# Performance work log

Measured on AMD Instinct MI355X. Metric: run time of the kernel, lower is better.

Reference implementation:

```python
import jax, jax.numpy as jnp
import numpy as np

N_NODES = 100000
N_EDGES = 1600000
K = 48

def setup_inputs() -> dict:
    key = jax.random.key(0)
    ks = jax.random.split(key, 6)
    x = jax.random.normal(ks[0], (N_NODES, K), dtype=jnp.float32)
    pos_edge_index = jax.random.randint(ks[1], (2, N_EDGES), 0, N_NODES, dtype=jnp.int64)
    neg_edge_index = jax.random.randint(ks[2], (2, N_EDGES), 0, N_NODES, dtype=jnp.int64)
    # nn.Linear-style init (uniform +-1/sqrt(fan_in))
    lim1 = 1.0 / np.sqrt(3 * K)
    W1 = jax.random.uniform(ks[3], (3 * K, 16), minval=-lim1, maxval=lim1, dtype=jnp.float32)
    b1 = jnp.zeros((16,), dtype=jnp.float32)
    lim2 = 1.0 / np.sqrt(16)
    W2 = jax.random.uniform(ks[4], (16, K), minval=-lim2, maxval=lim2, dtype=jnp.float32)
    b2 = jnp.zeros((K,), dtype=jnp.float32)
    return {"x": x, "pos_edge_index": pos_edge_index, "neg_edge_index": neg_edge_index,
            "W1": W1, "b1": b1, "W2": W2, "b2": b2}

def _scatter_add_mp(x, edge_index):
    # PyG MessagePassing(aggr='add'), message = x_j:
    # gather source-node features and scatter-add into target nodes.
    src, dst = edge_index[0], edge_index[1]
    msgs = x[src]  # [E, k]
    return jax.ops.segment_sum(msgs, dst, num_segments=x.shape[0])  # [N, k]

def reference(x, pos_edge_index, neg_edge_index, W1, b1, W2, b2):
    x_pos = _scatter_add_mp(x, pos_edge_index)
    x_neg = _scatter_add_mp(x, neg_edge_index)
    out_cat = jnp.concatenate([x, x_pos, x_neg], axis=1)  # [N, 3k]
    h = jnp.tanh(out_cat @ W1 + b1)                        # [N, 16]
    C = h @ W2 + b2                                        # [N, k]
    return jax.nn.softmax(C, axis=1)
```

## Files before the change

kernel.cpp:

```cpp
#include <hip/hip_runtime.h>
#include <hip/hip_fp16.h>
#include <math.h>

#define NN 100000
#define NE 1600000
#define KF 48
#define NEDGE_ALL (2 * NE)

#define BKT_NODES 128
#define NBKT_PER  782
#define NBKT      1564
#define PACK_EPB  4096
#define NPB       782
#define OT2       1566
#define CAP2      2432
#define KSTG      10

typedef _Float16 half2v __attribute__((ext_vector_type(2)));
typedef _Float16 half4v __attribute__((ext_vector_type(4)));
typedef _Float16 half8v __attribute__((ext_vector_type(8)));

#if defined(__has_builtin)
#if __has_builtin(__builtin_amdgcn_fdot2)
#define HAVE_FDOT2 1
#endif
#endif

__device__ __forceinline__ void acc_pair(float& ax, float& ay, half2v v)
{
#ifdef HAVE_FDOT2
    ax = __builtin_amdgcn_fdot2(v, (half2v){(_Float16)1.f, (_Float16)0.f}, ax, false);
    ay = __builtin_amdgcn_fdot2(v, (half2v){(_Float16)0.f, (_Float16)1.f}, ay, false);
#else
    ax += (float)v.x;
    ay += (float)v.y;
#endif
}

__global__ __launch_bounds__(512) void pack_kernel(
    const float* __restrict__ x,
    const int* __restrict__ ei_pos,
    const int* __restrict__ ei_neg,
    const float* __restrict__ W1,
    const float* __restrict__ b1,
    unsigned short* __restrict__ offT,
    unsigned* __restrict__ plist,
    float* __restrict__ za,
    __half* __restrict__ zbh,
    __half* __restrict__ zch)
{
    __shared__ int cnt[NBKT];
    __shared__ int ps[391];
    __shared__ unsigned stage[PACK_EPB];
    __shared__ float sW1[144 * 16];
    __shared__ float sb1[16];

    const int t = threadIdx.x;
    for (int i = t; i < 144 * 16; i += 512) sW1[i] = W1[i];
    if (t < 16) sb1[t] = b1[t];
    for (int i = t; i < NBKT; i += 512) cnt[i] = 0;
    __syncthreads();

    {
        const int n = blockIdx.x * 512 + t;
        if (n < NN + 2) {
            float aA[16], aB[16], aC[16];
#pragma unroll
            for (int j = 0; j < 16; ++j) { aA[j] = sb1[j]; aB[j] = 0.f; aC[j] = 0.f; }
            if (n < NN) {
                const float4* __restrict__ x4 = (const float4*)(x + (long)n * KF);
                for (int i4 = 0; i4 < 12; ++i4) {
                    float4 v = x4[i4];
                    float vv[4] = {v.x, v.y, v.z, v.w};
#pragma unroll
                    for (int c = 0; c < 4; ++c) {
                        const int f = i4 * 4 + c;
                        const float* wA = &sW1[f * 16];
                        const float* wB = &sW1[(48 + f) * 16];
                        const float* wC = &sW1[(96 + f) * 16];
                        const float s = vv[c];
#pragma unroll
                        for (int j = 0; j < 16; ++j) {
                            aA[j] += s * wA[j];
                            aB[j] += s * wB[j];
                            aC[j] += s * wC[j];
                        }
                    }
                }
                float4* za4 = (float4*)(za + (long)n * 16);
#pragma unroll
                for (int j4 = 0; j4 < 4; ++j4)
                    za4[j4] = make_float4(aA[4*j4], aA[4*j4+1], aA[4*j4+2], aA[4*j4+3]);
            }
            half8v hb0, hb1, hc0, hc1;
#pragma unroll
            for (int j = 0; j < 8; ++j) {
                hb0[j] = (_Float16)aB[j];     hb1[j] = (_Float16)aB[8 + j];
                hc0[j] = (_Float16)aC[j];     hc1[j] = (_Float16)aC[8 + j];
            }
            half8v* zb8 = (half8v*)zbh;
            half8v* zc8 = (half8v*)zch;
            zb8[(long)n * 2 + 0] = hb0;  zb8[(long)n * 2 + 1] = hb1;
            zc8[(long)n * 2 + 0] = hc0;  zc8[(long)n * 2 + 1] = hc1;
        }
    }

    unsigned pk[8];
    int bk[8];
    const int blockBase = blockIdx.x * PACK_EPB;
#pragma unroll
    for (int j = 0; j < 8; ++j) {
        int e = blockBase + j * 512 + t;
        bk[j] = -1;
        if (e < NEDGE_ALL) {
            int list = e >= NE;
            int ee = list ? e - NE : e;
            const int* ei = list ? ei_neg : ei_pos;
            int src = ei[ee];
            int dst = ei[NE + ee];
            int b = list * NBKT_PER + (dst >> 7);
            bk[j] = b;
            pk[j] = ((unsigned)(dst & 127) << 17) | (unsigned)src;
            atomicAdd(&cnt[b], 1);
        }
    }
    __syncthreads();

    int s0 = 0, s1 = 0, s2 = 0, s3 = 0;
    if (t < 391) {
        s0 = cnt[4 * t]; s1 = cnt[4 * t + 1]; s2 = cnt[4 * t + 2]; s3 = cnt[4 * t + 3];
        ps[t] = s0 + s1 + s2 + s3;
    }
    __syncthreads();
    for (int d = 1; d < 391; d <<= 1) {
        int v = (t < 391 && t >= d) ? ps[t - d] : 0;
        __syncthreads();
        if (t < 391) ps[t] += v;
        __syncthreads();
    }
    unsigned short* myrow = offT + (long)blockIdx.x * OT2;
    if (t < 391) {
        int base = t ? ps[t - 1] : 0;
        int o0 = base, o1 = o0 + s0, o2 = o1 + s1, o3 = o2 + s2;
        myrow[4 * t]     = (unsigned short)o0;
        myrow[4 * t + 1] = (unsigned short)o1;
        myrow[4 * t + 2] = (unsigned short)o2;
        myrow[4 * t + 3] = (unsigned short)o3;
        cnt[4 * t] = o0; cnt[4 * t + 1] = o1; cnt[4 * t + 2] = o2; cnt[4 * t + 3] = o3;
    }
    if (t == 390) myrow[NBKT] = (unsigned short)ps[390];
    __syncthreads();

#pragma unroll
    for (int j = 0; j < 8; ++j) {
        if (bk[j] >= 0) {
            int slot = atomicAdd(&cnt[bk[j]], 1);
            stage[slot] = pk[j];
        }
    }
    __syncthreads();

    {
        const uint4* __restrict__ st4 = (const uint4*)stage;
        uint4* __restrict__ out4 = (uint4*)(plist + (long)blockIdx.x * PACK_EPB);
#pragma unroll
        for (int j = 0; j < 2; ++j)
            out4[j * 512 + t] = st4[j * 512 + t];
    }
}

__global__ __launch_bounds__(256) void gather_kernel(
    const __half* __restrict__ zbh,
    const __half* __restrict__ zch,
    const unsigned* __restrict__ plist,
    const unsigned short* __restrict__ offT,
    float* __restrict__ hpos,
    float* __restrict__ hneg)
{
    __shared__ unsigned srt[CAP2];
    __shared__ int rb[NPB + 2];
    __shared__ unsigned short rsL[NPB];
    __shared__ int tmp[196];
    __shared__ int nh[BKT_NODES];
    __shared__ int starts[BKT_NODES];
    __shared__ int ends[BKT_NODES];
    __shared__ int cur2[BKT_NODES];

    const int b = blockIdx.x;
    const int t = threadIdx.x;

    for (int r = t; r < NPB; r += 256) {
        int s = offT[(long)r * OT2 + b];
        int e = offT[(long)r * OT2 + b + 1];
        rsL[r] = (unsigned short)s;
        srt[r] = (unsigned)(e - s);
    }
    if (t < BKT_NODES) nh[t] = 0;
    __syncthreads();

    int s0 = 0, s1 = 0, s2 = 0, s3 = 0;
    if (t < 196) {
        int i0 = 4 * t;
        s0 = (i0     < NPB) ? (int)srt[i0]     : 0;
        s1 = (i0 + 1 < NPB) ? (int)srt[i0 + 1] : 0;
        s2 = (i0 + 2 < NPB) ? (int)srt[i0 + 2] : 0;
        s3 = (i0 + 3 < NPB) ? (int)srt[i0 + 3] : 0;
        tmp[t] = s0 + s1 + s2 + s3;
    }
    __syncthreads();
    for (int d = 1; d < 196; d <<= 1) {
        int v = (t < 196 && t >= d) ? tmp[t - d] : 0;
        __syncthreads();
        if (t < 196) tmp[t] += v;
        __syncthreads();
    }
    if (t < 196) {
        int base = t ? tmp[t - 1] : 0;
        int i0 = 4 * t;
        if (i0     <= NPB) rb[i0]     = base;
        if (i0 + 1 <= NPB) rb[i0 + 1] = base + s0;
        if (i0 + 2 <= NPB) rb[i0 + 2] = base + s0 + s1;
        if (i0 + 3 <= NPB) rb[i0 + 3] = base + s0 + s1 + s2;
    }
    __syncthreads();
    int cb = rb[NPB];
    if (cb > CAP2) cb = CAP2;

    unsigned held[KSTG];
#pragma unroll
    for (int k = 0; k < KSTG; ++k) {
        int i = t + k * 256;
        held[k] = 0;
        if (i < cb) {
            int lo = 0, hi = NPB - 1;
#pragma unroll
            for (int it = 0; it < 10; ++it) {
                int mid = (lo + hi + 1) >> 1;
                bool ge = (rb[mid] <= i);
                lo = ge ? mid : lo;
                hi = ge ? hi : mid - 1;
            }
            unsigned p = plist[(long)lo * PACK_EPB + rsL[lo] + (i - rb[lo])];
            held[k] = p;
            atomicAdd(&nh[p >> 17], 1);
        }
    }
    __syncthreads();

    for (int d = 1; d < BKT_NODES; d <<= 1) {
        int v = 0;
        if (t < BKT_NODES && t >= d) v = nh[t - d];
        __syncthreads();
        if (t < BKT_NODES) nh[t] += v;
        __syncthreads();
    }
    if (t < BKT_NODES) {
        int e_ = min(nh[t], CAP2);
        int s_ = t ? min(nh[t - 1], CAP2) : 0;
        starts[t] = s_;
        ends[t] = e_;
        cur2[t] = s_;
    }
    __syncthreads();

#pragma unroll
    for (int k = 0; k < KSTG; ++k) {
        int i = t + k * 256;
        if (i < cb) {
            unsigned p = held[k];
            int slot = atomicAdd(&cur2[p >> 17], 1);
            if (slot < CAP2) srt[slot] = p;
        }
    }
    __syncthreads();

    const int wave = t >> 6, lane = t & 63;
    const int g = lane >> 2;
    const int sub = lane & 3;
    const int list = b >= NBKT_PER;
    const int nb = list ? b - NBKT_PER : b;
    float* o = list ? hneg : hpos;
    const half4v* __restrict__ z4 = (const half4v*)(list ? zch : zbh);

    for (int n = wave; n < BKT_NODES; n += 4) {
        int gn = nb * BKT_NODES + n;
        if (gn >= NN) continue;
        int s = starts[n], e = ends[n];
        float a0 = 0.f, a1 = 0.f, a2 = 0.f, a3 = 0.f;
        for (int j = s; j < e; j += 16) {
            int i0 = j + g;
            int q = (i0 < e) ? (int)(srt[i0 < CAP2 ? i0 : 0] & 0x1FFFFu) : NN;
            half4v v = z4[q * 4 + sub];
            acc_pair(a0, a1, (half2v){v.x, v.y});
            acc_pair(a2, a3, (half2v){v.z, v.w});
        }
        a0 += __shfl_xor(a0, 4); a0 += __shfl_xor(a0, 8); a0 += __shfl_xor(a0, 16); a0 += __shfl_xor(a0, 32);
        a1 += __shfl_xor(a1, 4); a1 += __shfl_xor(a1, 8); a1 += __shfl_xor(a1, 16); a1 += __shfl_xor(a1, 32);
        a2 += __shfl_xor(a2, 4); a2 += __shfl_xor(a2, 8); a2 += __shfl_xor(a2, 16); a2 += __shfl_xor(a2, 32);
        a3 += __shfl_xor(a3, 4); a3 += __shfl_xor(a3, 8); a3 += __shfl_xor(a3, 16); a3 += __shfl_xor(a3, 32);
        if (g == 0) {
            float4* o4 = (float4*)o;
            o4[(long)gn * 4 + sub] = make_float4(a0, a1, a2, a3);
        }
    }
}

__global__ __launch_bounds__(256) void mlp2_kernel(
    const float* __restrict__ za,
    const float* __restrict__ hpos,
    const float* __restrict__ hneg,
    const float* __restrict__ W2,
    const float* __restrict__ b2,
    float* __restrict__ out)
{
    __shared__ float sW2[16 * 48];
    __shared__ float sb2[48];
    for (int i = threadIdx.x; i < 16 * 48; i += 256) sW2[i] = W2[i];
    if (threadIdx.x < 48) sb2[threadIdx.x] = b2[threadIdx.x];
    __syncthreads();

    const int n = blockIdx.x * 256 + threadIdx.x;
    if (n >= NN) return;

    const float4* A = (const float4*)(za   + (long)n * 16);
    const float4* P = (const float4*)(hpos + (long)n * 16);
    const float4* Q = (const float4*)(hneg + (long)n * 16);
    float h[16];
#pragma unroll
    for (int j4 = 0; j4 < 4; ++j4) {
        float4 a = A[j4], p = P[j4], q = Q[j4];
        h[4 * j4 + 0] = tanhf(a.x + p.x + q.x);
        h[4 * j4 + 1] = tanhf(a.y + p.y + q.y);
        h[4 * j4 + 2] = tanhf(a.z + p.z + q.z);
        h[4 * j4 + 3] = tanhf(a.w + p.w + q.w);
    }

    float C[KF];
#pragma unroll
    for (int k = 0; k < KF; ++k) C[k] = sb2[k];
    for (int j = 0; j < 16; ++j) {
        const float hv = h[j];
        const float* w = &sW2[j * KF];
#pragma unroll
        for (int k = 0; k < KF; ++k) C[k] += hv * w[k];
    }

    float m = C[0];
#pragma unroll
    for (int k = 1; k < KF; ++k) m = fmaxf(m, C[k]);
    float ssum = 0.f;
#pragma unroll
    for (int k = 0; k < KF; ++k) { C[k] = expf(C[k] - m); ssum += C[k]; }
    const float inv = 1.0f / ssum;

    float4* po = (float4*)(out + (long)n * KF);
#pragma unroll
    for (int k4 = 0; k4 < 12; ++k4)
        po[k4] = make_float4(C[4*k4] * inv, C[4*k4+1] * inv, C[4*k4+2] * inv, C[4*k4+3] * inv);
}

__global__ __launch_bounds__(256) void scatter2_kernel(
    const float* __restrict__ x,
    const int* __restrict__ ei_pos,
    const int* __restrict__ ei_neg,
    float* acc_pos,
    float* acc_neg)
{
    const int list = blockIdx.y;
    const int* ei = list ? ei_neg : ei_pos;
    float* acc = list ? acc_neg : acc_pos;

    long t = (long)blockIdx.x * blockDim.x + threadIdx.x;
    const long total = (long)NE * 12;
    if (t >= total) return;

    int e = (int)(t / 12);
    int r = (int)(t - (long)e * 12);
    int k4 = r * 4;

    int src = ei[e];
    int dst = ei[NE + e];

    const float4 v = *(const float4*)(x + (long)src * KF + k4);
    float* p = acc + (long)dst * KF + k4;

    unsafeAtomicAdd(p + 0, v.x);
    unsafeAtomicAdd(p + 1, v.y);
    unsafeAtomicAdd(p + 2, v.z);
    unsafeAtomicAdd(p + 3, v.w);
}

__global__ __launch_bounds__(256) void mlp_softmax_kernel(
    const float* __restrict__ x,
    const float* xpos,
    const float* __restrict__ xneg,
    const float* __restrict__ W1,
    const float* __restrict__ b1,
    const float* __restrict__ W2,
    const float* __restrict__ b2,
    float* out)
{
    __shared__ float sW1[144 * 16];
    __shared__ float sW2[16 * 48];
    __shared__ float sb1[16];
    __shared__ float sb2[48];

    for (int i = threadIdx.x; i < 144 * 16; i += blockDim.x) sW1[i] = W1[i];
    for (int i = threadIdx.x; i < 16 * 48;  i += blockDim.x) sW2[i] = W2[i];
    if (threadIdx.x < 16) sb1[threadIdx.x] = b1[threadIdx.x];
    if (threadIdx.x < 48) sb2[threadIdx.x] = b2[threadIdx.x];
    __syncthreads();

    const int n = blockIdx.x * blockDim.x + threadIdx.x;
    if (n >= NN) return;

    float h[16];
#pragma unroll
    for (int j = 0; j < 16; ++j) h[j] = sb1[j];

    const float* srcs[3];
    srcs[0] = x    + (long)n * KF;
    srcs[1] = xpos + (long)n * KF;
    srcs[2] = xneg + (long)n * KF;

    for (int s = 0; s < 3; ++s) {
        const float* px = srcs[s];
        for (int i = 0; i < KF; ++i) {
            const float v = px[i];
            const float* w = &sW1[(s * KF + i) * 16];
#pragma unroll
            for (int j = 0; j < 16; ++j) h[j] += v * w[j];
        }
    }
#pragma unroll
    for (int j = 0; j < 16; ++j) h[j] = tanhf(h[j]);

    float C[KF];
#pragma unroll
    for (int k = 0; k < KF; ++k) C[k] = sb2[k];
    for (int j = 0; j < 16; ++j) {
        const float hv = h[j];
        const float* w = &sW2[j * KF];
#pragma unroll
        for (int k = 0; k < KF; ++k) C[k] += hv * w[k];
    }

    float m = C[0];
#pragma unroll
    for (int k = 1; k < KF; ++k) m = fmaxf(m, C[k]);
    float ssum = 0.f;
#pragma unroll
    for (int k = 0; k < KF; ++k) { C[k] = expf(C[k] - m); ssum += C[k]; }
    const float inv = 1.0f / ssum;

    float* po = out + (long)n * KF;
#pragma unroll
    for (int k = 0; k < KF; ++k) po[k] = C[k] * inv;
}

extern "C" void kernel_launch(void* const* d_in, const int* in_sizes, int n_in,
                              void* d_out, int out_size, void* d_ws, size_t ws_size,
                              hipStream_t stream)
{
    const float* x      = (const float*)d_in[0];
    const int*   ei_pos = (const int*)  d_in[1];
    const int*   ei_neg = (const int*)  d_in[2];
    const float* W1     = (const float*)d_in[3];
    const float* b1     = (const float*)d_in[4];
    const float* W2     = (const float*)d_in[5];
    const float* b2     = (const float*)d_in[6];

    float* out = (float*)d_out;

    const size_t h_bytes     = (size_t)NN * 16 * sizeof(float);
    const size_t za_bytes    = (size_t)NN * 16 * sizeof(float);
    const size_t zh_bytes    = (size_t)(NN + 2) * 16 * sizeof(__half);
    const size_t plist_bytes = (size_t)NPB * PACK_EPB * sizeof(unsigned);
    const size_t offT_bytes  = (size_t)NPB * OT2 * sizeof(unsigned short);

    size_t off = 0;
    char* ws = (char*)d_ws;
    float*          hpos  = (float*)(ws + off);          off += h_bytes;
    float*          hneg  = (float*)(ws + off);          off += h_bytes;
    float*          za    = (float*)(ws + off);          off += za_bytes;
    __half*         zbh   = (__half*)(ws + off);         off += zh_bytes;
    __half*         zch   = (__half*)(ws + off);         off += zh_bytes;
    unsigned*       plist = (unsigned*)(ws + off);       off += plist_bytes;
    unsigned short* offT  = (unsigned short*)(ws + off); off += offT_bytes;
    const size_t needed = off;

    if (ws_size >= needed) {
        pack_kernel<<<NPB, 512, 0, stream>>>(x, ei_pos, ei_neg, W1, b1, offT, plist, za, zbh, zch);
        gather_kernel<<<NBKT, 256, 0, stream>>>(zbh, zch, plist, offT, hpos, hneg);
        mlp2_kernel<<<(NN + 255) / 256, 256, 0, stream>>>(za, hpos, hneg, W2, b2, out);
    } else {
        float* xpos = (float*)d_out;
        float* xneg = (float*)d_ws;
        const size_t acc_bytes = (size_t)NN * KF * sizeof(float);
        hipMemsetAsync(xpos, 0, acc_bytes, stream);
        hipMemsetAsync(xneg, 0, acc_bytes, stream);
        const long total = (long)NE * 12;
        dim3 grid((unsigned)((total + 255) / 256), 2, 1);
        scatter2_kernel<<<grid, 256, 0, stream>>>(x, ei_pos, ei_neg, xpos, xneg);
        mlp_softmax_kernel<<<(NN + 255) / 256, 256, 0, stream>>>(x, xpos, xneg, W1, b1, W2, b2, out);
    }
}
```

Baseline: 204.2 us.

## Pack 16K edges per block to shrink per-bucket offset table rows

The pack kernel now handles 16384 edges per block instead of 4096, so there are 196 pack blocks rather than 782. Because the staging buffer would not fit in LDS, it is written out in two halves. The gather kernel now reads 196 offset rows per bucket instead of 782, which simplifies its prefix scan and shortens its binary search. In exchange, each pack block holds 32 edges per thread in registers, issues more LDS atomics, and adds extra barriers. Fewer pack blocks may also leave the GPU underused, and offsets stored as unsigned short could overflow if one bucket's count within a block reached 65536.

```diff
diff --git a/kernel.cpp b/kernel.cpp
--- a/kernel.cpp
+++ b/kernel.cpp
@@ -10,8 +10,9 @@
 #define BKT_NODES 128
 #define NBKT_PER  782
 #define NBKT      1564
-#define PACK_EPB  4096
-#define NPB       782
+#define PACK_EPB  16384
+#define STG_HALF  8192
+#define NPB       196
 #define OT2       1566
 #define CAP2      2432
 #define KSTG      10
@@ -51,7 +52,7 @@
 {
     __shared__ int cnt[NBKT];
     __shared__ int ps[391];
-    __shared__ unsigned stage[PACK_EPB];
+    __shared__ unsigned stage[STG_HALF];
     __shared__ float sW1[144 * 16];
     __shared__ float sb1[16];
 
@@ -105,11 +106,11 @@
         }
     }
 
-    unsigned pk[8];
-    int bk[8];
+    unsigned pk[32];
+    int bk[32];
     const int blockBase = blockIdx.x * PACK_EPB;
 #pragma unroll
-    for (int j = 0; j < 8; ++j) {
+    for (int j = 0; j < 32; ++j) {
         int e = blockBase + j * 512 + t;
         bk[j] = -1;
         if (e < NEDGE_ALL) {
@@ -152,19 +153,37 @@
     __syncthreads();
 
 #pragma unroll
-    for (int j = 0; j < 8; ++j) {
-        if (bk[j] >= 0) {
-            int slot = atomicAdd(&cnt[bk[j]], 1);
-            stage[slot] = pk[j];
-        }
-    }
-    __syncthreads();
-
+    for (int j = 0; j < 32; ++j) {
+        if (bk[j] >= 0)
+            bk[j] = atomicAdd(&cnt[bk[j]], 1);
+    }
+
+#pragma unroll
+    for (int j = 0; j < 32; ++j) {
+        if (bk[j] >= 0 && bk[j] < STG_HALF)
+            stage[bk[j]] = pk[j];
+    }
+    __syncthreads();
     {
         const uint4* __restrict__ st4 = (const uint4*)stage;
         uint4* __restrict__ out4 = (uint4*)(plist + (long)blockIdx.x * PACK_EPB);
 #pragma unroll
-        for (int j = 0; j < 2; ++j)
+        for (int j = 0; j < 4; ++j)
+            out4[j * 512 + t] = st4[j * 512 + t];
+    }
+    __syncthreads();
+
+#pragma unroll
+    for (int j = 0; j < 32; ++j) {
+        if (bk[j] >= STG_HALF)
+            stage[bk[j] - STG_HALF] = pk[j];
+    }
+    __syncthreads();
+    {
+        const uint4* __restrict__ st4 = (const uint4*)stage;
+        uint4* __restrict__ out4 = (uint4*)(plist + (long)blockIdx.x * PACK_EPB + STG_HALF);
+#pragma unroll
+        for (int j = 0; j < 4; ++j)
             out4[j * 512 + t] = st4[j * 512 + t];
     }
 }
@@ -179,8 +198,8 @@
 {
     __shared__ unsigned srt[CAP2];
     __shared__ int rb[NPB + 2];
+    __shared__ int sc[NPB];
     __shared__ unsigned short rsL[NPB];
-    __shared__ int tmp[196];
     __shared__ int nh[BKT_NODES];
     __shared__ int starts[BKT_NODES];
     __shared__ int ends[BKT_NODES];
@@ -189,39 +208,23 @@
     const int b = blockIdx.x;
     const int t = threadIdx.x;
 
-    for (int r = t; r < NPB; r += 256) {
-        int s = offT[(long)r * OT2 + b];
-        int e = offT[(long)r * OT2 + b + 1];
-        rsL[r] = (unsigned short)s;
-        srt[r] = (unsigned)(e - s);
+    if (t < NPB) {
+        int s = offT[(long)t * OT2 + b];
+        int e = offT[(long)t * OT2 + b + 1];
+        rsL[t] = (unsigned short)s;
+        sc[t] = e - s;
     }
     if (t < BKT_NODES) nh[t] = 0;
     __syncthreads();
 
-    int s0 = 0, s1 = 0, s2 = 0, s3 = 0;
-    if (t < 196) {
-        int i0 = 4 * t;
-        s0 = (i0     < NPB) ? (int)srt[i0]     : 0;
-        s1 = (i0 + 1 < NPB) ? (int)srt[i0 + 1] : 0;
-        s2 = (i0 + 2 < NPB) ? (int)srt[i0 + 2] : 0;
-        s3 = (i0 + 3 < NPB) ? (int)srt[i0 + 3] : 0;
-        tmp[t] = s0 + s1 + s2 + s3;
-    }
-    __syncthreads();
-    for (int d = 1; d < 196; d <<= 1) {
-        int v = (t < 196 && t >= d) ? tmp[t - d] : 0;
+    for (int d = 1; d < NPB; d <<= 1) {
+        int v = (t < NPB && t >= d) ? sc[t - d] : 0;
         __syncthreads();
-        if (t < 196) tmp[t] += v;
+        if (t < NPB) sc[t] += v;
         __syncthreads();
     }
-    if (t < 196) {
-        int base = t ? tmp[t - 1] : 0;
-        int i0 = 4 * t;
-        if (i0     <= NPB) rb[i0]     = base;
-        if (i0 + 1 <= NPB) rb[i0 + 1] = base + s0;
-        if (i0 + 2 <= NPB) rb[i0 + 2] = base + s0 + s1;
-        if (i0 + 3 <= NPB) rb[i0 + 3] = base + s0 + s1 + s2;
-    }
+    if (t < NPB) rb[t + 1] = sc[t];
+    if (t == 0) rb[0] = 0;
     __syncthreads();
     int cb = rb[NPB];
     if (cb > CAP2) cb = CAP2;
@@ -234,7 +237,7 @@
         if (i < cb) {
             int lo = 0, hi = NPB - 1;
 #pragma unroll
-            for (int it = 0; it < 10; ++it) {
+            for (int it = 0; it < 8; ++it) {
                 int mid = (lo + hi + 1) >> 1;
                 bool ge = (rb[mid] <= i);
                 lo = ge ? mid : lo;
```

Result: no change. 207.2 us (+1.5%).
